# Kernel optimization log

Hardware: AMD Instinct MI355X
Metric: run time of the kernel (lower is better)

Reference implementation:

```python
import jax, jax.numpy as jnp
import numpy as np

T, H, E, I, TOPK = 2048, 1024, 8, 2048, 2


def setup_inputs() -> dict:
    key = jax.random.key(0)
    k1, k2, k3, k4 = jax.random.split(key, 4)
    hidden_states = jax.random.normal(k1, (T, H), dtype=jnp.float32)
    router_logits = jax.random.normal(k2, (T, E), dtype=jnp.float32)
    # w13: merged gate+up projection [E, 2I, H]; w2: down projection [E, H, I]
    w13_weight = jax.random.normal(k3, (E, 2 * I, H), dtype=jnp.float32) * 0.02
    w2_weight = jax.random.normal(k4, (E, H, I), dtype=jnp.float32) * 0.02
    return {
        "hidden_states": hidden_states,
        "router_logits": router_logits,
        "w13_weight": w13_weight,
        "w2_weight": w2_weight,
        "top_k": TOPK,
    }


def reference(hidden_states, router_logits, w13_weight, w2_weight, top_k):
    num_experts = router_logits.shape[-1]
    # --- top-k routing (softmax -> top_k -> renormalize) ---
    probs = jax.nn.softmax(router_logits, axis=-1)           # [T, E]
    topk_w, topk_ids = jax.lax.top_k(probs, top_k)           # [T, K]
    topk_w = topk_w / jnp.sum(topk_w, axis=-1, keepdims=True)
    # per-token combine weight for each expert: [T, E]
    onehot = jax.nn.one_hot(topk_ids, num_experts, dtype=hidden_states.dtype)  # [T, K, E]
    combine_w = jnp.einsum("tk,tke->te", topk_w, onehot)
    # --- grouped expert GEMMs (gated SiLU MLP) ---
    gu = jnp.einsum("th,eih->tei", hidden_states, w13_weight)  # [T, E, 2I]
    inter = w13_weight.shape[1] // 2
    gate, up = gu[..., :inter], gu[..., inter:]
    act = jax.nn.silu(gate) * up                               # [T, E, I]
    y = jnp.einsum("tei,ehi->teh", act, w2_weight)             # [T, E, H]
    # --- combine ---
    out = jnp.einsum("teh,te->th", y, combine_w)               # [T, H]
    return out
```

## Files before the change

### kernel.cpp

```cpp
#include <hip/hip_runtime.h>

#define T_ 2048
#define H_ 1024
#define E_ 8
#define I_ 2048

typedef short bf16x8 __attribute__((ext_vector_type(8)));
typedef float f32x4 __attribute__((ext_vector_type(4)));
typedef unsigned short u16x8 __attribute__((ext_vector_type(8)));

__device__ __forceinline__ unsigned short f2bf(float f) {
  unsigned u = __builtin_bit_cast(unsigned, f);
  u += 0x7fffu + ((u >> 16) & 1u);
  return (unsigned short)(u >> 16);
}

__device__ __forceinline__ float bf2f(unsigned short h) {
  unsigned u = ((unsigned)h) << 16;
  return __builtin_bit_cast(float, u);
}

#define GLOAD_LDS16(g, l)                                                     \
  __builtin_amdgcn_global_load_lds(                                           \
      (const __attribute__((address_space(1))) unsigned int*)(g),             \
      (__attribute__((address_space(3))) unsigned int*)(l), 16, 0, 0)

__global__ __launch_bounds__(256) void cvt_kernel(const float* __restrict__ s,
                                                  unsigned short* __restrict__ d,
                                                  int n8) {
  int i = blockIdx.x * blockDim.x + threadIdx.x;
  if (i >= n8) return;
  const float4* s4 = (const float4*)s;
  float4 a = s4[2 * i], b = s4[2 * i + 1];
  u16x8 v;
  v[0] = f2bf(a.x); v[1] = f2bf(a.y); v[2] = f2bf(a.z); v[3] = f2bf(a.w);
  v[4] = f2bf(b.x); v[5] = f2bf(b.y); v[6] = f2bf(b.z); v[7] = f2bf(b.w);
  *(u16x8*)(d + (size_t)i * 8) = v;
}

__global__ void router_kernel(const float* __restrict__ logits,
                              int* __restrict__ cnt,
                              int* __restrict__ plist,
                              float* __restrict__ wlist) {
  int t = blockIdx.x * blockDim.x + threadIdx.x;
  if (t >= T_) return;
  float l[E_];
#pragma unroll
  for (int e = 0; e < E_; ++e) l[e] = logits[t * E_ + e];
  int i0 = 0;
#pragma unroll
  for (int e = 1; e < E_; ++e) if (l[e] > l[i0]) i0 = e;
  int i1 = (i0 == 0) ? 1 : 0;
#pragma unroll
  for (int e = 0; e < E_; ++e) if (e != i0 && l[e] > l[i1]) i1 = e;
  float w1 = 1.f / (1.f + __expf(l[i0] - l[i1]));
  float w0 = 1.f - w1;
  int s0 = atomicAdd(&cnt[i0], 1);
  plist[i0 * T_ + s0] = 2 * t;
  wlist[i0 * T_ + s0] = w0;
  int s1 = atomicAdd(&cnt[i1], 1);
  plist[i1 * T_ + s1] = 2 * t + 1;
  wlist[i1 * T_ + s1] = w1;
}

__global__ __launch_bounds__(256, 4) void gemm1_kernel(
    const unsigned short* __restrict__ hs_bf,
    const float* __restrict__ w13,
    const int* __restrict__ cnt, const int* __restrict__ plist,
    const float* __restrict__ wlist, unsigned short* __restrict__ act) {
  const int bid = blockIdx.x;
  const int e = bid & 7;
  const int mt = (bid >> 3) & 15;
  const int nt = bid >> 7;
  const int M = cnt[e];
  if (mt * 128 >= M) return;
  const int Mrem = M - mt * 128;
  const int n0 = nt * 64;

  __shared__ __align__(16) unsigned short As[2][128][32];
  __shared__ __align__(16) unsigned short Bs[128][32];

  const int tid = threadIdx.x;
  const int lane = tid & 63;
  const int wid = tid >> 6;
  const int wm = (wid >> 1) * 64;
  const int wn = (wid & 1) * 32;

  const unsigned short* aSrc0;
  const unsigned short* aSrc1;
  {
    int cg = ((lane & 3) ^ ((lane >> 3) & 3)) * 8;
#pragma unroll
    for (int i = 0; i < 2; ++i) {
      int r = wid * 32 + i * 16 + (lane >> 2);
      int idx = mt * 128 + ((r < Mrem) ? r : 0);
      int p = plist[e * T_ + idx];
      const unsigned short* s = hs_bf + (size_t)(p >> 1) * H_ + cg;
      if (i == 0) aSrc0 = s; else aSrc1 = s;
    }
  }
  const int rb = wid * 32 + (lane >> 1);
  const int wrow = (rb < 64) ? (e * 2 * I_ + n0 + rb)
                             : (e * 2 * I_ + I_ + n0 + (rb - 64));
  const float* bSrc = w13 + (size_t)wrow * H_ + (lane & 1) * 16;
  const int fb = (rb >> 1) & 3;
  unsigned short* bDst0 = &Bs[rb][((((lane & 1) << 1) | 0) ^ fb) * 8];
  unsigned short* bDst1 = &Bs[rb][((((lane & 1) << 1) | 1) ^ fb) * 8];

  const int rda = ((lane >> 4) ^ ((lane >> 1) & 3)) * 8;
  const int l15 = lane & 15;

  f32x4 accg[4][2] = {};
  f32x4 accu[4][2] = {};

  GLOAD_LDS16(aSrc0, &As[0][wid * 32][0]);
  GLOAD_LDS16(aSrc1, &As[0][wid * 32 + 16][0]);
  float4 b0 = *(const float4*)(bSrc + 0);
  float4 b1 = *(const float4*)(bSrc + 4);
  float4 b2 = *(const float4*)(bSrc + 8);
  float4 b3 = *(const float4*)(bSrc + 12);

#pragma unroll 1
  for (int kt = 0; kt < 32; ++kt) {
    const int cur = kt & 1;
    asm volatile("s_waitcnt vmcnt(0)" ::: "memory");
    {
      u16x8 lo, hi;
      lo[0] = f2bf(b0.x); lo[1] = f2bf(b0.y); lo[2] = f2bf(b0.z); lo[3] = f2bf(b0.w);
      lo[4] = f2bf(b1.x); lo[5] = f2bf(b1.y); lo[6] = f2bf(b1.z); lo[7] = f2bf(b1.w);
      hi[0] = f2bf(b2.x); hi[1] = f2bf(b2.y); hi[2] = f2bf(b2.z); hi[3] = f2bf(b2.w);
      hi[4] = f2bf(b3.x); hi[5] = f2bf(b3.y); hi[6] = f2bf(b3.z); hi[7] = f2bf(b3.w);
      *(u16x8*)bDst0 = lo;
      *(u16x8*)bDst1 = hi;
    }
    if (kt + 1 < 32) {
      GLOAD_LDS16(aSrc0 + (kt + 1) * 32, &As[cur ^ 1][wid * 32][0]);
      GLOAD_LDS16(aSrc1 + (kt + 1) * 32, &As[cur ^ 1][wid * 32 + 16][0]);
      b0 = *(const float4*)(bSrc + (kt + 1) * 32 + 0);
      b1 = *(const float4*)(bSrc + (kt + 1) * 32 + 4);
      b2 = *(const float4*)(bSrc + (kt + 1) * 32 + 8);
      b3 = *(const float4*)(bSrc + (kt + 1) * 32 + 12);
    }
    asm volatile("s_waitcnt lgkmcnt(0)" ::: "memory");
    __builtin_amdgcn_s_barrier();
    __builtin_amdgcn_sched_barrier(0);

    bf16x8 bg[2], bu[2];
#pragma unroll
    for (int ni = 0; ni < 2; ++ni) {
      bg[ni] = *(const bf16x8*)&Bs[wn + ni * 16 + l15][rda];
      bu[ni] = *(const bf16x8*)&Bs[64 + wn + ni * 16 + l15][rda];
    }
#pragma unroll
    for (int mi = 0; mi < 4; ++mi) {
      bf16x8 af = *(const bf16x8*)&As[cur][wm + mi * 16 + l15][rda];
#pragma unroll
      for (int ni = 0; ni < 2; ++ni) {
        accg[mi][ni] = __builtin_amdgcn_mfma_f32_16x16x32_bf16(af, bg[ni], accg[mi][ni], 0, 0, 0);
        accu[mi][ni] = __builtin_amdgcn_mfma_f32_16x16x32_bf16(af, bu[ni], accu[mi][ni], 0, 0, 0);
      }
    }
    __builtin_amdgcn_sched_barrier(0);
    __builtin_amdgcn_s_barrier();
  }

  const int lrow = lane >> 4, lcol = lane & 15;
#pragma unroll
  for (int mi = 0; mi < 4; ++mi) {
#pragma unroll
    for (int r = 0; r < 4; ++r) {
      int rl = wm + mi * 16 + lrow * 4 + r;
      if (rl < Mrem) {
        int rr = mt * 128 + rl;
        int p = plist[e * T_ + rr];
        float w = wlist[e * T_ + rr];
        unsigned short* dst = act + (size_t)p * I_ + n0;
#pragma unroll
        for (int ni = 0; ni < 2; ++ni) {
          float g = accg[mi][ni][r];
          float u = accu[mi][ni][r];
          float a = (g / (1.f + __expf(-g))) * u * w;
          dst[wn + ni * 16 + lcol] = f2bf(a);
        }
      }
    }
  }
}

__global__ __launch_bounds__(256, 4) void gemm2_kernel(
    const unsigned short* __restrict__ act,
    const float* __restrict__ w2,
    const int* __restrict__ cnt, const int* __restrict__ plist,
    unsigned short* __restrict__ part) {
  const int bid = blockIdx.x;
  const int e = bid & 7;
  const int mt = (bid >> 3) & 15;
  const int nt = (bid >> 7) & 7;
  const int kb = bid >> 10;
  const int M = cnt[e];
  if (mt * 128 >= M) return;
  const int Mrem = M - mt * 128;
  const int n0 = nt * 128;
  const int k0 = kb * 1024;

  __shared__ __align__(16) unsigned short As[2][128][32];
  __shared__ __align__(16) unsigned short Bs[128][32];

  const int tid = threadIdx.x;
  const int lane = tid & 63;
  const int wid = tid >> 6;
  const int wm = (wid >> 1) * 64;
  const int wn = (wid & 1) * 64;

  const unsigned short* aSrc0;
  const unsigned short* aSrc1;
  {
    int cg = ((lane & 3) ^ ((lane >> 3) & 3)) * 8;
#pragma unroll
    for (int i = 0; i < 2; ++i) {
      int r = wid * 32 + i * 16 + (lane >> 2);
      int idx = mt * 128 + ((r < Mrem) ? r : 0);
      int p = plist[e * T_ + idx];
      const unsigned short* s = act + (size_t)p * I_ + k0 + cg;
      if (i == 0) aSrc0 = s; else aSrc1 = s;
    }
  }
  const int rb = wid * 32 + (lane >> 1);
  const float* bSrc = w2 + ((size_t)e * H_ + n0 + rb) * I_ + k0 + (lane & 1) * 16;
  const int fb = (rb >> 1) & 3;
  unsigned short* bDst0 = &Bs[rb][((((lane & 1) << 1) | 0) ^ fb) * 8];
  unsigned short* bDst1 = &Bs[rb][((((lane & 1) << 1) | 1) ^ fb) * 8];

  const int rda = ((lane >> 4) ^ ((lane >> 1) & 3)) * 8;
  const int l15 = lane & 15;

  f32x4 acc[4][4] = {};

  GLOAD_LDS16(aSrc0, &As[0][wid * 32][0]);
  GLOAD_LDS16(aSrc1, &As[0][wid * 32 + 16][0]);
  float4 b0 = *(const float4*)(bSrc + 0);
  float4 b1 = *(const float4*)(bSrc + 4);
  float4 b2 = *(const float4*)(bSrc + 8);
  float4 b3 = *(const float4*)(bSrc + 12);

#pragma unroll 1
  for (int kt = 0; kt < 32; ++kt) {
    const int cur = kt & 1;
    asm volatile("s_waitcnt vmcnt(0)" ::: "memory");
    {
      u16x8 lo, hi;
      lo[0] = f2bf(b0.x); lo[1] = f2bf(b0.y); lo[2] = f2bf(b0.z); lo[3] = f2bf(b0.w);
      lo[4] = f2bf(b1.x); lo[5] = f2bf(b1.y); lo[6] = f2bf(b1.z); lo[7] = f2bf(b1.w);
      hi[0] = f2bf(b2.x); hi[1] = f2bf(b2.y); hi[2] = f2bf(b2.z); hi[3] = f2bf(b2.w);
      hi[4] = f2bf(b3.x); hi[5] = f2bf(b3.y); hi[6] = f2bf(b3.z); hi[7] = f2bf(b3.w);
      *(u16x8*)bDst0 = lo;
      *(u16x8*)bDst1 = hi;
    }
    if (kt + 1 < 32) {
      GLOAD_LDS16(aSrc0 + (kt + 1) * 32, &As[cur ^ 1][wid * 32][0]);
      GLOAD_LDS16(aSrc1 + (kt + 1) * 32, &As[cur ^ 1][wid * 32 + 16][0]);
      b0 = *(const float4*)(bSrc + (kt + 1) * 32 + 0);
      b1 = *(const float4*)(bSrc + (kt + 1) * 32 + 4);
      b2 = *(const float4*)(bSrc + (kt + 1) * 32 + 8);
      b3 = *(const float4*)(bSrc + (kt + 1) * 32 + 12);
    }
    asm volatile("s_waitcnt lgkmcnt(0)" ::: "memory");
    __builtin_amdgcn_s_barrier();
    __builtin_amdgcn_sched_barrier(0);

    bf16x8 bb[4];
#pragma unroll
    for (int ni = 0; ni < 4; ++ni)
      bb[ni] = *(const bf16x8*)&Bs[wn + ni * 16 + l15][rda];
#pragma unroll
    for (int mi = 0; mi < 4; ++mi) {
      bf16x8 af = *(const bf16x8*)&As[cur][wm + mi * 16 + l15][rda];
#pragma unroll
      for (int ni = 0; ni < 4; ++ni)
        acc[mi][ni] = __builtin_amdgcn_mfma_f32_16x16x32_bf16(af, bb[ni], acc[mi][ni], 0, 0, 0);
    }
    __builtin_amdgcn_sched_barrier(0);
    __builtin_amdgcn_s_barrier();
  }

  const int lrow = lane >> 4, lcol = lane & 15;
#pragma unroll
  for (int mi = 0; mi < 4; ++mi) {
#pragma unroll
    for (int r = 0; r < 4; ++r) {
      int rl = wm + mi * 16 + lrow * 4 + r;
      if (rl < Mrem) {
        int p = plist[e * T_ + mt * 128 + rl];
        unsigned short* dst = part + ((size_t)kb * 2 * T_ + p) * H_ + n0 + wn + lcol;
#pragma unroll
        for (int ni = 0; ni < 4; ++ni)
          dst[ni * 16] = f2bf(acc[mi][ni][r]);
      }
    }
  }
}

__global__ __launch_bounds__(256) void reduce_kernel(const unsigned short* __restrict__ part,
                                                     float* __restrict__ out) {
  int i = blockIdx.x * blockDim.x + threadIdx.x;
  int t = i >> 7;
  int c = (i & 127) << 3;
  float s[8] = {0.f, 0.f, 0.f, 0.f, 0.f, 0.f, 0.f, 0.f};
#pragma unroll
  for (int kb = 0; kb < 2; ++kb) {
#pragma unroll
    for (int pp = 0; pp < 2; ++pp) {
      u16x8 v = *(const u16x8*)(part + ((size_t)kb * 2 * T_ + 2 * t + pp) * H_ + c);
#pragma unroll
      for (int j = 0; j < 8; ++j) s[j] += bf2f(v[j]);
    }
  }
  float* o = out + (size_t)t * H_ + c;
  *(f32x4*)o = *(f32x4*)&s[0];
  *(f32x4*)(o + 4) = *(f32x4*)&s[4];
}

extern "C" void kernel_launch(void* const* d_in, const int* in_sizes, int n_in,
                              void* d_out, int out_size, void* d_ws, size_t ws_size,
                              hipStream_t stream) {
  const float* hs     = (const float*)d_in[0];
  const float* logits = (const float*)d_in[1];
  const float* w13    = (const float*)d_in[2];
  const float* w2     = (const float*)d_in[3];
  float* out = (float*)d_out;

  char* ws = (char*)d_ws;
  size_t off = 0;
  int* cnt = (int*)(ws + off);           off += 256;
  int* plist = (int*)(ws + off);         off += (size_t)E_ * T_ * 4;
  float* wlist = (float*)(ws + off);     off += (size_t)E_ * T_ * 4;
  unsigned short* act = (unsigned short*)(ws + off);   off += (size_t)2 * T_ * I_ * 2;
  unsigned short* hs_bf = (unsigned short*)(ws + off); off += (size_t)T_ * H_ * 2;
  unsigned short* part = (unsigned short*)(ws + off);  off += (size_t)2 * 2 * T_ * H_ * 2;

  hipMemsetAsync(cnt, 0, 256, stream);

  const int nHs = T_ * H_ / 8;
  cvt_kernel<<<(nHs + 255) / 256, 256, 0, stream>>>(hs, hs_bf, nHs);
  router_kernel<<<T_ / 256, 256, 0, stream>>>(logits, cnt, plist, wlist);

  gemm1_kernel<<<E_ * 16 * 32, 256, 0, stream>>>(hs_bf, w13, cnt, plist, wlist, act);
  gemm2_kernel<<<E_ * 16 * 8 * 2, 256, 0, stream>>>(act, w2, cnt, plist, part);
  reduce_kernel<<<T_ * H_ / 8 / 256, 256, 0, stream>>>(part, out);
}
```

Baseline: 195.0 us.

## Keep full-K weight slice resident in LDS and stream gathered activations from global

The gate/up GEMM is restructured into 512-thread blocks. Each block converts a 64-row by full-K slice of w13 to bf16 once into 128KB of LDS, then runs the whole K loop with no per-iteration barriers. Activation fragments are gathered straight from global memory into registers and double-buffered there, instead of being staged through LDS. Each block now covers up to 512 tokens per expert, so the fp32 weights are read from HBM far fewer times. The cost is one block per CU, uncoalesced 16-byte A gathers that depend on L2 hits, and a hard limit of 1024 tokens per expert, since only two M tiles are launched.

```diff
diff --git a/kernel.cpp b/kernel.cpp
--- a/kernel.cpp
+++ b/kernel.cpp
@@ -63,124 +63,114 @@
   wlist[i1 * T_ + s1] = w1;
 }
 
-__global__ __launch_bounds__(256, 4) void gemm1_kernel(
+__global__ __launch_bounds__(512, 1) void gemm1_kernel(
     const unsigned short* __restrict__ hs_bf,
     const float* __restrict__ w13,
     const int* __restrict__ cnt, const int* __restrict__ plist,
     const float* __restrict__ wlist, unsigned short* __restrict__ act) {
   const int bid = blockIdx.x;
   const int e = bid & 7;
-  const int mt = (bid >> 3) & 15;
-  const int nt = bid >> 7;
+  const int mt = (bid >> 3) & 1;
+  const int nt = bid >> 4;
   const int M = cnt[e];
-  if (mt * 128 >= M) return;
-  const int Mrem = M - mt * 128;
-  const int n0 = nt * 64;
-
-  __shared__ __align__(16) unsigned short As[2][128][32];
-  __shared__ __align__(16) unsigned short Bs[128][32];
+  const int m0 = mt * 512;
+  if (m0 >= M) return;
+  int Mloc = M - m0; if (Mloc > 512) Mloc = 512;
+  const int n0 = nt * 32;
+
+  __shared__ __align__(16) unsigned short Bs[64 * 1024];
 
   const int tid = threadIdx.x;
   const int lane = tid & 63;
   const int wid = tid >> 6;
-  const int wm = (wid >> 1) * 64;
-  const int wn = (wid & 1) * 32;
-
-  const unsigned short* aSrc0;
-  const unsigned short* aSrc1;
+  const int l15 = lane & 15;
+  const int q = lane >> 4;
+
   {
-    int cg = ((lane & 3) ^ ((lane >> 3) & 3)) * 8;
-#pragma unroll
-    for (int i = 0; i < 2; ++i) {
-      int r = wid * 32 + i * 16 + (lane >> 2);
-      int idx = mt * 128 + ((r < Mrem) ? r : 0);
-      int p = plist[e * T_ + idx];
-      const unsigned short* s = hs_bf + (size_t)(p >> 1) * H_ + cg;
-      if (i == 0) aSrc0 = s; else aSrc1 = s;
-    }
-  }
-  const int rb = wid * 32 + (lane >> 1);
-  const int wrow = (rb < 64) ? (e * 2 * I_ + n0 + rb)
-                             : (e * 2 * I_ + I_ + n0 + (rb - 64));
-  const float* bSrc = w13 + (size_t)wrow * H_ + (lane & 1) * 16;
-  const int fb = (rb >> 1) & 3;
-  unsigned short* bDst0 = &Bs[rb][((((lane & 1) << 1) | 0) ^ fb) * 8];
-  unsigned short* bDst1 = &Bs[rb][((((lane & 1) << 1) | 1) ^ fb) * 8];
-
-  const int rda = ((lane >> 4) ^ ((lane >> 1) & 3)) * 8;
-  const int l15 = lane & 15;
+    int r = tid >> 3;
+    int seg = tid & 7;
+    int wr = (r < 32) ? (e * 2 * I_ + n0 + r)
+                      : (e * 2 * I_ + I_ + n0 + (r - 32));
+    const float4* src = (const float4*)(w13 + (size_t)wr * H_ + seg * 128);
+    unsigned short* lrow = &Bs[r * 1024];
+    const int x = r & 7;
+#pragma unroll
+    for (int j = 0; j < 16; ++j) {
+      float4 a = src[2 * j], b = src[2 * j + 1];
+      u16x8 o;
+      o[0] = f2bf(a.x); o[1] = f2bf(a.y); o[2] = f2bf(a.z); o[3] = f2bf(a.w);
+      o[4] = f2bf(b.x); o[5] = f2bf(b.y); o[6] = f2bf(b.z); o[7] = f2bf(b.w);
+      int ck = seg * 16 + j;
+      *(u16x8*)&lrow[(ck ^ x) * 8] = o;
+    }
+  }
+
+  const unsigned short* aPtr[4];
+#pragma unroll
+  for (int mi = 0; mi < 4; ++mi) {
+    int rl = wid * 64 + mi * 16 + l15;
+    int idx = m0 + ((rl < Mloc) ? rl : 0);
+    int p = plist[e * T_ + idx] >> 1;
+    aPtr[mi] = hs_bf + (size_t)p * H_ + q * 8;
+  }
+  __syncthreads();
 
   f32x4 accg[4][2] = {};
   f32x4 accu[4][2] = {};
 
-  GLOAD_LDS16(aSrc0, &As[0][wid * 32][0]);
-  GLOAD_LDS16(aSrc1, &As[0][wid * 32 + 16][0]);
-  float4 b0 = *(const float4*)(bSrc + 0);
-  float4 b1 = *(const float4*)(bSrc + 4);
-  float4 b2 = *(const float4*)(bSrc + 8);
-  float4 b3 = *(const float4*)(bSrc + 12);
-
-#pragma unroll 1
+  bf16x8 aC0, aC1, aC2, aC3, aN0, aN1, aN2, aN3;
+  aC0 = *(const bf16x8*)(aPtr[0]);
+  aC1 = *(const bf16x8*)(aPtr[1]);
+  aC2 = *(const bf16x8*)(aPtr[2]);
+  aC3 = *(const bf16x8*)(aPtr[3]);
+
+#pragma unroll 2
   for (int kt = 0; kt < 32; ++kt) {
-    const int cur = kt & 1;
-    asm volatile("s_waitcnt vmcnt(0)" ::: "memory");
-    {
-      u16x8 lo, hi;
-      lo[0] = f2bf(b0.x); lo[1] = f2bf(b0.y); lo[2] = f2bf(b0.z); lo[3] = f2bf(b0.w);
-      lo[4] = f2bf(b1.x); lo[5] = f2bf(b1.y); lo[6] = f2bf(b1.z); lo[7] = f2bf(b1.w);
-      hi[0] = f2bf(b2.x); hi[1] = f2bf(b2.y); hi[2] = f2bf(b2.z); hi[3] = f2bf(b2.w);
-      hi[4] = f2bf(b3.x); hi[5] = f2bf(b3.y); hi[6] = f2bf(b3.z); hi[7] = f2bf(b3.w);
-      *(u16x8*)bDst0 = lo;
-      *(u16x8*)bDst1 = hi;
-    }
     if (kt + 1 < 32) {
-      GLOAD_LDS16(aSrc0 + (kt + 1) * 32, &As[cur ^ 1][wid * 32][0]);
-      GLOAD_LDS16(aSrc1 + (kt + 1) * 32, &As[cur ^ 1][wid * 32 + 16][0]);
-      b0 = *(const float4*)(bSrc + (kt + 1) * 32 + 0);
-      b1 = *(const float4*)(bSrc + (kt + 1) * 32 + 4);
-      b2 = *(const float4*)(bSrc + (kt + 1) * 32 + 8);
-      b3 = *(const float4*)(bSrc + (kt + 1) * 32 + 12);
-    }
-    asm volatile("s_waitcnt lgkmcnt(0)" ::: "memory");
-    __builtin_amdgcn_s_barrier();
-    __builtin_amdgcn_sched_barrier(0);
-
+      aN0 = *(const bf16x8*)(aPtr[0] + (kt + 1) * 32);
+      aN1 = *(const bf16x8*)(aPtr[1] + (kt + 1) * 32);
+      aN2 = *(const bf16x8*)(aPtr[2] + (kt + 1) * 32);
+      aN3 = *(const bf16x8*)(aPtr[3] + (kt + 1) * 32);
+    }
+    const int ck = kt * 4 + q;
     bf16x8 bg[2], bu[2];
 #pragma unroll
     for (int ni = 0; ni < 2; ++ni) {
-      bg[ni] = *(const bf16x8*)&Bs[wn + ni * 16 + l15][rda];
-      bu[ni] = *(const bf16x8*)&Bs[64 + wn + ni * 16 + l15][rda];
-    }
-#pragma unroll
-    for (int mi = 0; mi < 4; ++mi) {
-      bf16x8 af = *(const bf16x8*)&As[cur][wm + mi * 16 + l15][rda];
-#pragma unroll
-      for (int ni = 0; ni < 2; ++ni) {
-        accg[mi][ni] = __builtin_amdgcn_mfma_f32_16x16x32_bf16(af, bg[ni], accg[mi][ni], 0, 0, 0);
-        accu[mi][ni] = __builtin_amdgcn_mfma_f32_16x16x32_bf16(af, bu[ni], accu[mi][ni], 0, 0, 0);
-      }
-    }
-    __builtin_amdgcn_sched_barrier(0);
-    __builtin_amdgcn_s_barrier();
-  }
-
-  const int lrow = lane >> 4, lcol = lane & 15;
+      int rg = ni * 16 + l15;
+      int ru = 32 + rg;
+      bg[ni] = *(const bf16x8*)&Bs[rg * 1024 + ((ck ^ (rg & 7)) * 8)];
+      bu[ni] = *(const bf16x8*)&Bs[ru * 1024 + ((ck ^ (ru & 7)) * 8)];
+    }
+#pragma unroll
+    for (int ni = 0; ni < 2; ++ni) {
+      accg[0][ni] = __builtin_amdgcn_mfma_f32_16x16x32_bf16(aC0, bg[ni], accg[0][ni], 0, 0, 0);
+      accu[0][ni] = __builtin_amdgcn_mfma_f32_16x16x32_bf16(aC0, bu[ni], accu[0][ni], 0, 0, 0);
+      accg[1][ni] = __builtin_amdgcn_mfma_f32_16x16x32_bf16(aC1, bg[ni], accg[1][ni], 0, 0, 0);
+      accu[1][ni] = __builtin_amdgcn_mfma_f32_16x16x32_bf16(aC1, bu[ni], accu[1][ni], 0, 0, 0);
+      accg[2][ni] = __builtin_amdgcn_mfma_f32_16x16x32_bf16(aC2, bg[ni], accg[2][ni], 0, 0, 0);
+      accu[2][ni] = __builtin_amdgcn_mfma_f32_16x16x32_bf16(aC2, bu[ni], accu[2][ni], 0, 0, 0);
+      accg[3][ni] = __builtin_amdgcn_mfma_f32_16x16x32_bf16(aC3, bg[ni], accg[3][ni], 0, 0, 0);
+      accu[3][ni] = __builtin_amdgcn_mfma_f32_16x16x32_bf16(aC3, bu[ni], accu[3][ni], 0, 0, 0);
+    }
+    aC0 = aN0; aC1 = aN1; aC2 = aN2; aC3 = aN3;
+  }
+
 #pragma unroll
   for (int mi = 0; mi < 4; ++mi) {
 #pragma unroll
-    for (int r = 0; r < 4; ++r) {
-      int rl = wm + mi * 16 + lrow * 4 + r;
-      if (rl < Mrem) {
-        int rr = mt * 128 + rl;
-        int p = plist[e * T_ + rr];
-        float w = wlist[e * T_ + rr];
+    for (int rr = 0; rr < 4; ++rr) {
+      int rl = wid * 64 + mi * 16 + q * 4 + rr;
+      if (rl < Mloc) {
+        int idx = m0 + rl;
+        int p = plist[e * T_ + idx];
+        float w = wlist[e * T_ + idx];
         unsigned short* dst = act + (size_t)p * I_ + n0;
 #pragma unroll
         for (int ni = 0; ni < 2; ++ni) {
-          float g = accg[mi][ni][r];
-          float u = accu[mi][ni][r];
+          float g = accg[mi][ni][rr];
+          float u = accu[mi][ni][rr];
           float a = (g / (1.f + __expf(-g))) * u * w;
-          dst[wn + ni * 16 + lcol] = f2bf(a);
+          dst[ni * 16 + l15] = f2bf(a);
         }
       }
     }
@@ -344,7 +334,7 @@
   cvt_kernel<<<(nHs + 255) / 256, 256, 0, stream>>>(hs, hs_bf, nHs);
   router_kernel<<<T_ / 256, 256, 0, stream>>>(logits, cnt, plist, wlist);
 
-  gemm1_kernel<<<E_ * 16 * 32, 256, 0, stream>>>(hs_bf, w13, cnt, plist, wlist, act);
+  gemm1_kernel<<<64 * 2 * 8, 512, 0, stream>>>(hs_bf, w13, cnt, plist, wlist, act);
   gemm2_kernel<<<E_ * 16 * 8 * 2, 256, 0, stream>>>(act, w2, cnt, plist, part);
   reduce_kernel<<<T_ * H_ / 8 / 256, 256, 0, stream>>>(part, out);
 }
```

After: 273.1 us. 1.4x slower.
